# Performance work log

Hardware: AMD Instinct MI355X
Metric: run time of the kernel (lower is better)

Reference implementation:

```python
import jax, jax.numpy as jnp
import numpy as np

EPS = 1e-5

def _bn(x, g, b):
    # BatchNorm1d in training mode: stats over (batch, length) dims, biased var
    mean = jnp.mean(x, axis=(0, 2), keepdims=True)
    var = jnp.var(x, axis=(0, 2), keepdims=True)
    return (x - mean) * jax.lax.rsqrt(var + EPS) * g[None, :, None] + b[None, :, None]

def _conv1x1(x, w, b):
    # pointwise Conv1d: [B,C,T] x [O,C] -> [B,O,T]
    return jnp.einsum('bct,oc->bot', x, w) + b[None, :, None]

def setup_inputs() -> dict:
    key = jax.random.key(0)
    ks = jax.random.split(key, 4)
    B, C, T = 32, 1024, 2048
    x = jax.random.normal(ks[0], (B, C, T), dtype=jnp.float32)
    w1 = jax.random.normal(ks[1], (256, 1024), dtype=jnp.float32) * (1.0 / np.sqrt(1024))
    w2 = jax.random.normal(ks[2], (64, 256), dtype=jnp.float32) * (1.0 / np.sqrt(256))
    return {
        'x': x,
        'bn1_g': jnp.ones((1024,), jnp.float32), 'bn1_b': jnp.zeros((1024,), jnp.float32),
        'w1': w1, 'b1': jnp.zeros((256,), jnp.float32),
        'bn2_g': jnp.ones((256,), jnp.float32), 'bn2_b': jnp.zeros((256,), jnp.float32),
        'w2': w2, 'b2': jnp.zeros((64,), jnp.float32),
    }

def reference(x, bn1_g, bn1_b, w1, b1, bn2_g, bn2_b, w2, b2):
    # reduction layer: BN -> 1x1 conv -> ReLU (1024 -> 256)
    h = jax.nn.relu(_conv1x1(_bn(x, bn1_g, bn1_b), w1, b1))
    # out layer: BN -> 1x1 conv, no activation (256 -> 64)
    out = _conv1x1(_bn(h, bn2_g, bn2_b), w2, b2)
    o = out.shape[1]
    mu = out[:, : o // 2, :]
    logvar = out[:, o // 2 :, :]
    return (mu, logvar)
```

## Files before the change

kernel.cpp:

```cpp
#include <hip/hip_runtime.h>

#define B_  32
#define C1  1024
#define C2  256
#define T_  2048
#define EPSF 1e-5f
#define CPAD 72

typedef __attribute__((ext_vector_type(8))) short bf16x8;
typedef __attribute__((ext_vector_type(4))) float f32x4;

static __device__ __forceinline__ unsigned short f2bf(float f) {
    union { float f; unsigned u; } v; v.f = f;
    unsigned r = v.u + 0x7fffu + ((v.u >> 16) & 1u);
    return (unsigned short)(r >> 16);
}
static __device__ __forceinline__ void g2l16(const void* g, void* l) {
    __builtin_amdgcn_global_load_lds(
        (const __attribute__((address_space(1))) unsigned int*)g,
        (__attribute__((address_space(3))) unsigned int*)l, 16, 0, 0);
}

__global__ __launch_bounds__(256) void k_prep(const float* __restrict__ x,
        unsigned short* __restrict__ xT, float* __restrict__ psum, float* __restrict__ psq) {
    __shared__ unsigned short tile[64 * CPAD];
    __shared__ float red[256];
    int ct = blockIdx.x, b = blockIdx.y, tid = threadIdx.x;
    int c0 = ct * 64;
    int cl = tid >> 2, t4 = tid & 3;
    const float* xrow = x + (size_t)b * C1 * T_ + (size_t)(c0 + cl) * T_;
    float s = 0.f, sq = 0.f;
    for (int t0 = 0; t0 < T_; t0 += 64) {
        #pragma unroll
        for (int j = 0; j < 4; ++j) {
            int tl = j * 16 + t4 * 4;
            float4 v = *(const float4*)(xrow + t0 + tl);
            s  += v.x + v.y + v.z + v.w;
            sq += v.x * v.x + v.y * v.y + v.z * v.z + v.w * v.w;
            tile[(tl + 0) * CPAD + cl] = f2bf(v.x);
            tile[(tl + 1) * CPAD + cl] = f2bf(v.y);
            tile[(tl + 2) * CPAD + cl] = f2bf(v.z);
            tile[(tl + 3) * CPAD + cl] = f2bf(v.w);
        }
        __syncthreads();
        #pragma unroll
        for (int j = 0; j < 2; ++j) {
            int w = tid + j * 256;
            int tl = w >> 3, cu = w & 7;
            uint4 vv = *(const uint4*)&tile[tl * CPAD + cu * 8];
            *(uint4*)&xT[((size_t)b * T_ + t0 + tl) * C1 + c0 + cu * 8] = vv;
        }
        __syncthreads();
    }
    red[tid] = s; __syncthreads();
    if (tid < 64)
        psum[(size_t)b * C1 + c0 + tid] = red[4*tid] + red[4*tid+1] + red[4*tid+2] + red[4*tid+3];
    __syncthreads();
    red[tid] = sq; __syncthreads();
    if (tid < 64)
        psq[(size_t)b * C1 + c0 + tid]  = red[4*tid] + red[4*tid+1] + red[4*tid+2] + red[4*tid+3];
}

__global__ __launch_bounds__(256) void k_fold1(const float* __restrict__ w1,
        const float* __restrict__ b1, const float* __restrict__ g1, const float* __restrict__ bb1,
        const float* __restrict__ psum, const float* __restrict__ psq,
        unsigned short* __restrict__ w1e, float* __restrict__ b1e) {
    int o = blockIdx.x, tid = threadIdx.x;
    int c = tid * 4;
    float4 s = {0,0,0,0}, sq = {0,0,0,0};
    for (int b = 0; b < B_; ++b) {
        float4 a = *(const float4*)(psum + (size_t)b * C1 + c);
        float4 q = *(const float4*)(psq  + (size_t)b * C1 + c);
        s.x += a.x; s.y += a.y; s.z += a.z; s.w += a.w;
        sq.x += q.x; sq.y += q.y; sq.z += q.z; sq.w += q.w;
    }
    const float n = (float)(B_ * T_);
    float4 gg = *(const float4*)(g1 + c);
    float4 bv = *(const float4*)(bb1 + c);
    float m0 = s.x / n, m1 = s.y / n, m2 = s.z / n, m3 = s.w / n;
    float sc0 = gg.x * rsqrtf(sq.x / n - m0 * m0 + EPSF);
    float sc1 = gg.y * rsqrtf(sq.y / n - m1 * m1 + EPSF);
    float sc2 = gg.z * rsqrtf(sq.z / n - m2 * m2 + EPSF);
    float sc3 = gg.w * rsqrtf(sq.w / n - m3 * m3 + EPSF);
    float sh0 = bv.x - m0 * sc0, sh1 = bv.y - m1 * sc1;
    float sh2 = bv.z - m2 * sc2, sh3 = bv.w - m3 * sc3;
    float4 w = ((const float4*)(w1 + (size_t)o * C1))[tid];
    float p = w.x * sh0 + w.y * sh1 + w.z * sh2 + w.w * sh3;
    uint2 pk;
    pk.x = (unsigned)f2bf(w.x * sc0) | ((unsigned)f2bf(w.y * sc1) << 16);
    pk.y = (unsigned)f2bf(w.z * sc2) | ((unsigned)f2bf(w.w * sc3) << 16);
    *((uint2*)(w1e + (size_t)o * C1 + c)) = pk;
    __shared__ float rs[256];
    rs[tid] = p; __syncthreads();
    for (int off = 128; off > 0; off >>= 1) {
        if (tid < off) rs[tid] += rs[tid + off];
        __syncthreads();
    }
    if (tid == 0) b1e[o] = b1[o] + rs[0];
}

__global__ __launch_bounds__(256, 2) void k_gemm1(const unsigned short* __restrict__ xT,
        const unsigned short* __restrict__ w1e, const float* __restrict__ b1e,
        unsigned short* __restrict__ hT, float* __restrict__ p2s, float* __restrict__ p2q) {
    __shared__ unsigned short sA[256 * 32];
    __shared__ unsigned short sB[128 * 32];
    int bn = blockIdx.x, b = blockIdx.y;
    int tid = threadIdx.x;
    int wave = tid >> 6, lane = tid & 63;
    int wm = wave >> 1, wn = wave & 1;
    int l15 = lane & 15, q = lane >> 4;
    f32x4 acc[8][4] = {};
    const unsigned short* xblk = xT + ((size_t)b * T_ + (size_t)bn * 128) * C1;

    for (int k0 = 0; k0 < C1; k0 += 32) {
        #pragma unroll
        for (int i = 0; i < 4; ++i) {
            int idx = (wave * 4 + i) * 64 + lane;
            int row = idx >> 2, cq = idx & 3;
            g2l16(w1e + (size_t)row * C1 + k0 + cq * 8, &sA[(wave * 4 + i) * 512]);
        }
        #pragma unroll
        for (int i = 0; i < 2; ++i) {
            int idx = (wave * 2 + i) * 64 + lane;
            int row = idx >> 2, cq = idx & 3;
            g2l16(xblk + (size_t)row * C1 + k0 + cq * 8, &sB[(wave * 2 + i) * 512]);
        }
        __syncthreads();
        bf16x8 bfr[4];
        #pragma unroll
        for (int ni = 0; ni < 4; ++ni)
            bfr[ni] = *((const bf16x8*)&sB[(wn * 64 + ni * 16 + l15) * 32 + q * 8]);
        #pragma unroll
        for (int mi = 0; mi < 8; ++mi) {
            bf16x8 af = *((const bf16x8*)&sA[(wm * 128 + mi * 16 + l15) * 32 + q * 8]);
            #pragma unroll
            for (int ni = 0; ni < 4; ++ni)
                acc[mi][ni] = __builtin_amdgcn_mfma_f32_16x16x32_bf16(af, bfr[ni], acc[mi][ni], 0, 0, 0);
        }
        __syncthreads();
    }
    int obase = wm * 128;
    int tbase = bn * 128 + wn * 64;
    int prow = (b * 16 + bn) * 2 + wn;
    #pragma unroll
    for (int mi = 0; mi < 8; ++mi) {
        int og = obase + mi * 16 + q * 4;
        float4 bias = *(const float4*)&b1e[og];
        float s0 = 0, s1 = 0, s2 = 0, s3 = 0, q0 = 0, q1 = 0, q2 = 0, q3 = 0;
        #pragma unroll
        for (int ni = 0; ni < 4; ++ni) {
            int t = tbase + ni * 16 + l15;
            float v0 = fmaxf(acc[mi][ni][0] + bias.x, 0.f);
            float v1 = fmaxf(acc[mi][ni][1] + bias.y, 0.f);
            float v2 = fmaxf(acc[mi][ni][2] + bias.z, 0.f);
            float v3 = fmaxf(acc[mi][ni][3] + bias.w, 0.f);
            s0 += v0; q0 += v0 * v0;  s1 += v1; q1 += v1 * v1;
            s2 += v2; q2 += v2 * v2;  s3 += v3; q3 += v3 * v3;
            uint2 pk;
            pk.x = (unsigned)f2bf(v0) | ((unsigned)f2bf(v1) << 16);
            pk.y = (unsigned)f2bf(v2) | ((unsigned)f2bf(v3) << 16);
            *(uint2*)&hT[((size_t)b * T_ + t) * C2 + og] = pk;
        }
        #pragma unroll
        for (int m = 1; m <= 8; m <<= 1) {
            s0 += __shfl_xor(s0, m); s1 += __shfl_xor(s1, m);
            s2 += __shfl_xor(s2, m); s3 += __shfl_xor(s3, m);
            q0 += __shfl_xor(q0, m); q1 += __shfl_xor(q1, m);
            q2 += __shfl_xor(q2, m); q3 += __shfl_xor(q3, m);
        }
        if (l15 == 0) {
            *(float4*)&p2s[(size_t)prow * C2 + og] = make_float4(s0, s1, s2, s3);
            *(float4*)&p2q[(size_t)prow * C2 + og] = make_float4(q0, q1, q2, q3);
        }
    }
}

__global__ __launch_bounds__(256) void k_fold2(const float* __restrict__ w2,
        const float* __restrict__ b2, const float* __restrict__ g2, const float* __restrict__ bb2,
        const float* __restrict__ p2s, const float* __restrict__ p2q,
        unsigned short* __restrict__ w2e, float* __restrict__ b2e) {
    int o = blockIdx.x, tid = threadIdx.x;
    float s = 0.f, sq = 0.f;
    for (int r = 0; r < 1024; ++r) {
        s  += p2s[(size_t)r * C2 + tid];
        sq += p2q[(size_t)r * C2 + tid];
    }
    const float n = (float)(B_ * T_);
    float mean = s / n;
    float sc = g2[tid] * rsqrtf(sq / n - mean * mean + EPSF);
    float sh = bb2[tid] - mean * sc;
    float w = w2[(size_t)o * C2 + tid];
    float p = w * sh;
    w2e[(size_t)o * C2 + tid] = f2bf(w * sc);
    __shared__ float rs[256];
    rs[tid] = p; __syncthreads();
    for (int off = 128; off > 0; off >>= 1) {
        if (tid < off) rs[tid] += rs[tid + off];
        __syncthreads();
    }
    if (tid == 0) b2e[o] = b2[o] + rs[0];
}

__global__ __launch_bounds__(256) void k_gemm2(const unsigned short* __restrict__ hT,
        const unsigned short* __restrict__ w2e, const float* __restrict__ b2e,
        float* __restrict__ out) {
    __shared__ unsigned short sA[64 * 32];
    __shared__ unsigned short sB[128 * 32];
    int bn = blockIdx.x, b = blockIdx.y;
    int tid = threadIdx.x;
    int wave = tid >> 6, lane = tid & 63;
    int l15 = lane & 15, q = lane >> 4;
    f32x4 acc[4][2] = {};
    const unsigned short* hblk = hT + ((size_t)b * T_ + (size_t)bn * 128) * C2;

    for (int k0 = 0; k0 < C2; k0 += 32) {
        {
            int idx = wave * 64 + lane;
            int row = idx >> 2, cq = idx & 3;
            g2l16(w2e + (size_t)row * C2 + k0 + cq * 8, &sA[wave * 512]);
        }
        #pragma unroll
        for (int i = 0; i < 2; ++i) {
            int idx = (wave * 2 + i) * 64 + lane;
            int row = idx >> 2, cq = idx & 3;
            g2l16(hblk + (size_t)row * C2 + k0 + cq * 8, &sB[(wave * 2 + i) * 512]);
        }
        __syncthreads();
        bf16x8 af[4], bfr[2];
        #pragma unroll
        for (int mi = 0; mi < 4; ++mi)
            af[mi] = *((const bf16x8*)&sA[(mi * 16 + l15) * 32 + q * 8]);
        #pragma unroll
        for (int ni = 0; ni < 2; ++ni)
            bfr[ni] = *((const bf16x8*)&sB[(wave * 32 + ni * 16 + l15) * 32 + q * 8]);
        #pragma unroll
        for (int mi = 0; mi < 4; ++mi)
            #pragma unroll
            for (int ni = 0; ni < 2; ++ni)
                acc[mi][ni] = __builtin_amdgcn_mfma_f32_16x16x32_bf16(af[mi], bfr[ni], acc[mi][ni], 0, 0, 0);
        __syncthreads();
    }
    int tbase = bn * 128 + wave * 32;
    #pragma unroll
    for (int mi = 0; mi < 4; ++mi) {
        #pragma unroll
        for (int reg = 0; reg < 4; ++reg) {
            int o = mi * 16 + q * 4 + reg;
            float bias = b2e[o];
            size_t base = (o < 32)
                ? ((size_t)b * 32 * T_ + (size_t)o * T_)
                : (2097152u + (size_t)b * 32 * T_ + (size_t)(o - 32) * T_);
            #pragma unroll
            for (int ni = 0; ni < 2; ++ni) {
                int t = tbase + ni * 16 + l15;
                out[base + t] = acc[mi][ni][reg] + bias;
            }
        }
    }
}

extern "C" void kernel_launch(void* const* d_in, const int* in_sizes, int n_in,
                              void* d_out, int out_size, void* d_ws, size_t ws_size,
                              hipStream_t stream) {
    const float* x   = (const float*)d_in[0];
    const float* g1  = (const float*)d_in[1];
    const float* bb1 = (const float*)d_in[2];
    const float* w1  = (const float*)d_in[3];
    const float* b1  = (const float*)d_in[4];
    const float* g2  = (const float*)d_in[5];
    const float* bb2 = (const float*)d_in[6];
    const float* w2  = (const float*)d_in[7];
    const float* b2  = (const float*)d_in[8];
    float* out = (float*)d_out;

    char* ws = (char*)d_ws;
    float* b1e  = (float*)(ws + 0);
    float* b2e  = (float*)(ws + 4096);
    float* psum = (float*)(ws + 8192);
    float* psq  = (float*)(ws + 139264);
    float* p2s  = (float*)(ws + 270336);
    float* p2q  = (float*)(ws + 1318912);
    unsigned short* w1e = (unsigned short*)(ws + 2367488);
    unsigned short* w2e = (unsigned short*)(ws + 2891776);
    unsigned short* xT  = (unsigned short*)(ws + 2924544);
    unsigned short* hT  = (unsigned short*)(ws + 2924544 + 134217728);

    k_prep <<<dim3(16, 32), dim3(256), 0, stream>>>(x, xT, psum, psq);
    k_fold1<<<dim3(256),    dim3(256), 0, stream>>>(w1, b1, g1, bb1, psum, psq, w1e, b1e);
    k_gemm1<<<dim3(16, 32), dim3(256), 0, stream>>>(xT, w1e, b1e, hT, p2s, p2q);
    k_fold2<<<dim3(64),     dim3(256), 0, stream>>>(w2, b2, g2, bb2, p2s, p2q, w2e, b2e);
    k_gemm2<<<dim3(16, 32), dim3(256), 0, stream>>>(hT, w2e, b2e, out);
}
```

Measured before the change: 536.2 us.

## Double-buffer GEMM1 LDS tiles and precompute BN statistics in dedicated kernels

GEMM1 now stages the next K tile into a second LDS buffer while computing on the current one, overlapping global-to-LDS loads with MFMA work. BatchNorm scale/shift are computed once per channel in new bnstat kernels instead of being recomputed redundantly in every fold block, and the second-layer partial stats are stored channel-major so they can be reduced with coalesced loads. Block reductions switch to wave shuffles. Costs are doubled LDS usage and two extra kernel launches.

```diff
diff --git a/kernel.cpp b/kernel.cpp
--- a/kernel.cpp
+++ b/kernel.cpp
@@ -61,49 +61,49 @@
         psq[(size_t)b * C1 + c0 + tid]  = red[4*tid] + red[4*tid+1] + red[4*tid+2] + red[4*tid+3];
 }
 
+__global__ __launch_bounds__(256) void k_bnstat1(const float* __restrict__ psum,
+        const float* __restrict__ psq, const float* __restrict__ g1,
+        const float* __restrict__ bb1, float* __restrict__ sc1, float* __restrict__ sh1) {
+    int c = blockIdx.x * 256 + threadIdx.x;
+    float s = 0.f, q = 0.f;
+    for (int b = 0; b < B_; ++b) {
+        s += psum[(size_t)b * C1 + c];
+        q += psq[(size_t)b * C1 + c];
+    }
+    const float n = (float)(B_ * T_);
+    float m = s / n;
+    float sc = g1[c] * rsqrtf(q / n - m * m + EPSF);
+    sc1[c] = sc;
+    sh1[c] = bb1[c] - m * sc;
+}
+
 __global__ __launch_bounds__(256) void k_fold1(const float* __restrict__ w1,
-        const float* __restrict__ b1, const float* __restrict__ g1, const float* __restrict__ bb1,
-        const float* __restrict__ psum, const float* __restrict__ psq,
-        unsigned short* __restrict__ w1e, float* __restrict__ b1e) {
+        const float* __restrict__ b1, const float* __restrict__ sc1,
+        const float* __restrict__ sh1, unsigned short* __restrict__ w1e,
+        float* __restrict__ b1e) {
     int o = blockIdx.x, tid = threadIdx.x;
     int c = tid * 4;
-    float4 s = {0,0,0,0}, sq = {0,0,0,0};
-    for (int b = 0; b < B_; ++b) {
-        float4 a = *(const float4*)(psum + (size_t)b * C1 + c);
-        float4 q = *(const float4*)(psq  + (size_t)b * C1 + c);
-        s.x += a.x; s.y += a.y; s.z += a.z; s.w += a.w;
-        sq.x += q.x; sq.y += q.y; sq.z += q.z; sq.w += q.w;
-    }
-    const float n = (float)(B_ * T_);
-    float4 gg = *(const float4*)(g1 + c);
-    float4 bv = *(const float4*)(bb1 + c);
-    float m0 = s.x / n, m1 = s.y / n, m2 = s.z / n, m3 = s.w / n;
-    float sc0 = gg.x * rsqrtf(sq.x / n - m0 * m0 + EPSF);
-    float sc1 = gg.y * rsqrtf(sq.y / n - m1 * m1 + EPSF);
-    float sc2 = gg.z * rsqrtf(sq.z / n - m2 * m2 + EPSF);
-    float sc3 = gg.w * rsqrtf(sq.w / n - m3 * m3 + EPSF);
-    float sh0 = bv.x - m0 * sc0, sh1 = bv.y - m1 * sc1;
-    float sh2 = bv.z - m2 * sc2, sh3 = bv.w - m3 * sc3;
-    float4 w = ((const float4*)(w1 + (size_t)o * C1))[tid];
-    float p = w.x * sh0 + w.y * sh1 + w.z * sh2 + w.w * sh3;
+    float4 w  = ((const float4*)(w1 + (size_t)o * C1))[tid];
+    float4 sc = *(const float4*)(sc1 + c);
+    float4 sh = *(const float4*)(sh1 + c);
+    float p = w.x * sh.x + w.y * sh.y + w.z * sh.z + w.w * sh.w;
     uint2 pk;
-    pk.x = (unsigned)f2bf(w.x * sc0) | ((unsigned)f2bf(w.y * sc1) << 16);
-    pk.y = (unsigned)f2bf(w.z * sc2) | ((unsigned)f2bf(w.w * sc3) << 16);
+    pk.x = (unsigned)f2bf(w.x * sc.x) | ((unsigned)f2bf(w.y * sc.y) << 16);
+    pk.y = (unsigned)f2bf(w.z * sc.z) | ((unsigned)f2bf(w.w * sc.w) << 16);
     *((uint2*)(w1e + (size_t)o * C1 + c)) = pk;
-    __shared__ float rs[256];
-    rs[tid] = p; __syncthreads();
-    for (int off = 128; off > 0; off >>= 1) {
-        if (tid < off) rs[tid] += rs[tid + off];
-        __syncthreads();
-    }
-    if (tid == 0) b1e[o] = b1[o] + rs[0];
+    int wave = tid >> 6, lane = tid & 63;
+    for (int m = 1; m < 64; m <<= 1) p += __shfl_xor(p, m);
+    __shared__ float rs[4];
+    if (lane == 0) rs[wave] = p;
+    __syncthreads();
+    if (tid == 0) b1e[o] = b1[o] + rs[0] + rs[1] + rs[2] + rs[3];
 }
 
 __global__ __launch_bounds__(256, 2) void k_gemm1(const unsigned short* __restrict__ xT,
         const unsigned short* __restrict__ w1e, const float* __restrict__ b1e,
         unsigned short* __restrict__ hT, float* __restrict__ p2s, float* __restrict__ p2q) {
-    __shared__ unsigned short sA[256 * 32];
-    __shared__ unsigned short sB[128 * 32];
+    __shared__ unsigned short sA[2][256 * 32];
+    __shared__ unsigned short sB[2][128 * 32];
     int bn = blockIdx.x, b = blockIdx.y;
     int tid = threadIdx.x;
     int wave = tid >> 6, lane = tid & 63;
@@ -112,32 +112,39 @@
     f32x4 acc[8][4] = {};
     const unsigned short* xblk = xT + ((size_t)b * T_ + (size_t)bn * 128) * C1;
 
-    for (int k0 = 0; k0 < C1; k0 += 32) {
+    auto stage = [&](int buf, int k0) {
         #pragma unroll
         for (int i = 0; i < 4; ++i) {
             int idx = (wave * 4 + i) * 64 + lane;
             int row = idx >> 2, cq = idx & 3;
-            g2l16(w1e + (size_t)row * C1 + k0 + cq * 8, &sA[(wave * 4 + i) * 512]);
+            g2l16(w1e + (size_t)row * C1 + k0 + cq * 8, &sA[buf][(wave * 4 + i) * 512]);
         }
         #pragma unroll
         for (int i = 0; i < 2; ++i) {
             int idx = (wave * 2 + i) * 64 + lane;
             int row = idx >> 2, cq = idx & 3;
-            g2l16(xblk + (size_t)row * C1 + k0 + cq * 8, &sB[(wave * 2 + i) * 512]);
-        }
-        __syncthreads();
+            g2l16(xblk + (size_t)row * C1 + k0 + cq * 8, &sB[buf][(wave * 2 + i) * 512]);
+        }
+    };
+
+    stage(0, 0);
+    __syncthreads();
+    int cur = 0;
+    for (int kt = 0; kt < 32; ++kt) {
+        if (kt < 31) stage(cur ^ 1, (kt + 1) * 32);
         bf16x8 bfr[4];
         #pragma unroll
         for (int ni = 0; ni < 4; ++ni)
-            bfr[ni] = *((const bf16x8*)&sB[(wn * 64 + ni * 16 + l15) * 32 + q * 8]);
+            bfr[ni] = *((const bf16x8*)&sB[cur][(wn * 64 + ni * 16 + l15) * 32 + q * 8]);
         #pragma unroll
         for (int mi = 0; mi < 8; ++mi) {
-            bf16x8 af = *((const bf16x8*)&sA[(wm * 128 + mi * 16 + l15) * 32 + q * 8]);
+            bf16x8 af = *((const bf16x8*)&sA[cur][(wm * 128 + mi * 16 + l15) * 32 + q * 8]);
             #pragma unroll
             for (int ni = 0; ni < 4; ++ni)
                 acc[mi][ni] = __builtin_amdgcn_mfma_f32_16x16x32_bf16(af, bfr[ni], acc[mi][ni], 0, 0, 0);
         }
         __syncthreads();
+        cur ^= 1;
     }
     int obase = wm * 128;
     int tbase = bn * 128 + wn * 64;
@@ -169,36 +176,56 @@
             q2 += __shfl_xor(q2, m); q3 += __shfl_xor(q3, m);
         }
         if (l15 == 0) {
-            *(float4*)&p2s[(size_t)prow * C2 + og] = make_float4(s0, s1, s2, s3);
-            *(float4*)&p2q[(size_t)prow * C2 + og] = make_float4(q0, q1, q2, q3);
-        }
+            p2s[(size_t)(og + 0) * 1024 + prow] = s0;
+            p2s[(size_t)(og + 1) * 1024 + prow] = s1;
+            p2s[(size_t)(og + 2) * 1024 + prow] = s2;
+            p2s[(size_t)(og + 3) * 1024 + prow] = s3;
+            p2q[(size_t)(og + 0) * 1024 + prow] = q0;
+            p2q[(size_t)(og + 1) * 1024 + prow] = q1;
+            p2q[(size_t)(og + 2) * 1024 + prow] = q2;
+            p2q[(size_t)(og + 3) * 1024 + prow] = q3;
+        }
+    }
+}
+
+__global__ __launch_bounds__(256) void k_bnstat2(const float* __restrict__ p2s,
+        const float* __restrict__ p2q, const float* __restrict__ g2,
+        const float* __restrict__ bb2, float* __restrict__ sc2, float* __restrict__ sh2) {
+    int c = blockIdx.x, tid = threadIdx.x;
+    float4 a  = *(const float4*)(p2s + (size_t)c * 1024 + tid * 4);
+    float4 qv = *(const float4*)(p2q + (size_t)c * 1024 + tid * 4);
+    float s = a.x + a.y + a.z + a.w;
+    float q = qv.x + qv.y + qv.z + qv.w;
+    for (int m = 1; m < 64; m <<= 1) { s += __shfl_xor(s, m); q += __shfl_xor(q, m); }
+    __shared__ float rs[4], rq[4];
+    int wave = tid >> 6, lane = tid & 63;
+    if (lane == 0) { rs[wave] = s; rq[wave] = q; }
+    __syncthreads();
+    if (tid == 0) {
+        s = rs[0] + rs[1] + rs[2] + rs[3];
+        q = rq[0] + rq[1] + rq[2] + rq[3];
+        const float n = (float)(B_ * T_);
+        float m0 = s / n;
+        float sc = g2[c] * rsqrtf(q / n - m0 * m0 + EPSF);
+        sc2[c] = sc;
+        sh2[c] = bb2[c] - m0 * sc;
     }
 }
 
 __global__ __launch_bounds__(256) void k_fold2(const float* __restrict__ w2,
-        const float* __restrict__ b2, const float* __restrict__ g2, const float* __restrict__ bb2,
-        const float* __restrict__ p2s, const float* __restrict__ p2q,
-        unsigned short* __restrict__ w2e, float* __restrict__ b2e) {
+        const float* __restrict__ b2, const float* __restrict__ sc2,
+        const float* __restrict__ sh2, unsigned short* __restrict__ w2e,
+        float* __restrict__ b2e) {
     int o = blockIdx.x, tid = threadIdx.x;
-    float s = 0.f, sq = 0.f;
-    for (int r = 0; r < 1024; ++r) {
-        s  += p2s[(size_t)r * C2 + tid];
-        sq += p2q[(size_t)r * C2 + tid];
-    }
-    const float n = (float)(B_ * T_);
-    float mean = s / n;
-    float sc = g2[tid] * rsqrtf(sq / n - mean * mean + EPSF);
-    float sh = bb2[tid] - mean * sc;
     float w = w2[(size_t)o * C2 + tid];
-    float p = w * sh;
-    w2e[(size_t)o * C2 + tid] = f2bf(w * sc);
-    __shared__ float rs[256];
-    rs[tid] = p; __syncthreads();
-    for (int off = 128; off > 0; off >>= 1) {
-        if (tid < off) rs[tid] += rs[tid + off];
-        __syncthreads();
-    }
-    if (tid == 0) b2e[o] = b2[o] + rs[0];
+    w2e[(size_t)o * C2 + tid] = f2bf(w * sc2[tid]);
+    float p = w * sh2[tid];
+    int wave = tid >> 6, lane = tid & 63;
+    for (int m = 1; m < 64; m <<= 1) p += __shfl_xor(p, m);
+    __shared__ float rs[4];
+    if (lane == 0) rs[wave] = p;
+    __syncthreads();
+    if (tid == 0) b2e[o] = b2[o] + rs[0] + rs[1] + rs[2] + rs[3];
 }
 
 __global__ __launch_bounds__(256) void k_gemm2(const unsigned short* __restrict__ hT,
@@ -282,12 +309,18 @@
     float* p2q  = (float*)(ws + 1318912);
     unsigned short* w1e = (unsigned short*)(ws + 2367488);
     unsigned short* w2e = (unsigned short*)(ws + 2891776);
-    unsigned short* xT  = (unsigned short*)(ws + 2924544);
-    unsigned short* hT  = (unsigned short*)(ws + 2924544 + 134217728);
-
-    k_prep <<<dim3(16, 32), dim3(256), 0, stream>>>(x, xT, psum, psq);
-    k_fold1<<<dim3(256),    dim3(256), 0, stream>>>(w1, b1, g1, bb1, psum, psq, w1e, b1e);
-    k_gemm1<<<dim3(16, 32), dim3(256), 0, stream>>>(xT, w1e, b1e, hT, p2s, p2q);
-    k_fold2<<<dim3(64),     dim3(256), 0, stream>>>(w2, b2, g2, bb2, p2s, p2q, w2e, b2e);
-    k_gemm2<<<dim3(16, 32), dim3(256), 0, stream>>>(hT, w2e, b2e, out);
-}
+    float* sc1 = (float*)(ws + 2924544);
+    float* sh1 = (float*)(ws + 2928640);
+    float* sc2 = (float*)(ws + 2932736);
+    float* sh2 = (float*)(ws + 2933760);
+    unsigned short* xT  = (unsigned short*)(ws + 2934784);
+    unsigned short* hT  = (unsigned short*)(ws + 2934784 + 134217728);
+
+    k_prep   <<<dim3(16, 32), dim3(256), 0, stream>>>(x, xT, psum, psq);
+    k_bnstat1<<<dim3(4),      dim3(256), 0, stream>>>(psum, psq, g1, bb1, sc1, sh1);
+    k_fold1  <<<dim3(256),    dim3(256), 0, stream>>>(w1, b1, sc1, sh1, w1e, b1e);
+    k_gemm1  <<<dim3(16, 32), dim3(256), 0, stream>>>(xT, w1e, b1e, hT, p2s, p2q);
+    k_bnstat2<<<dim3(256),    dim3(256), 0, stream>>>(p2s, p2q, g2, bb2, sc2, sh2);
+    k_fold2  <<<dim3(64),     dim3(256), 0, stream>>>(w2, b2, sc2, sh2, w2e, b2e);
+    k_gemm2  <<<dim3(16, 32), dim3(256), 0, stream>>>(hT, w2e, b2e, out);
+}
```

Result: faster. 507.1 us (-5.4%).
